# Kernel optimization log

Measured on AMD Instinct MI355X. Metric: run time of the kernel, lower is better.

The kernel has to match this reference:

```python
import jax, jax.numpy as jnp
import numpy as np

EMB_DIM = 256
ATTN_DIM = 64
B, K = 16384, 64


def setup_inputs() -> dict:
    key = jax.random.key(0)
    ks = jax.random.split(key, 7)
    center = jax.random.normal(ks[0], (B, EMB_DIM), dtype=jnp.float32)
    neigh_embs = jax.random.normal(ks[1], (B, K, EMB_DIM), dtype=jnp.float32)
    ppi_weights = jax.random.uniform(ks[2], (B, K), dtype=jnp.float32)
    # learned params (Linear stores weight as [out, in]; we keep that layout)
    Wq = jax.random.normal(ks[3], (ATTN_DIM, EMB_DIM), dtype=jnp.float32) / np.sqrt(EMB_DIM)
    Wk = jax.random.normal(ks[4], (ATTN_DIM, EMB_DIM), dtype=jnp.float32) / np.sqrt(EMB_DIM)
    # xavier_uniform for W_gate: limit = sqrt(6/(fan_in+fan_out))
    lim = np.sqrt(6.0 / (2 * EMB_DIM + EMB_DIM))
    Wgate = jax.random.uniform(ks[5], (EMB_DIM, 2 * EMB_DIM), minval=-lim, maxval=lim, dtype=jnp.float32)
    bgate = jnp.zeros((EMB_DIM,), dtype=jnp.float32)
    return {"center": center, "neigh_embs": neigh_embs, "ppi_weights": ppi_weights,
            "Wq": Wq, "Wk": Wk, "Wgate": Wgate, "bgate": bgate}


def reference(center, neigh_embs, ppi_weights, Wq, Wk, Wgate, bgate):
    scale = ATTN_DIM ** -0.5
    q = center @ Wq.T                                   # [B, a]
    k = jnp.einsum('bkd,ad->bka', neigh_embs, Wk)        # [B, K, a]
    logits = jnp.einsum('ba,bka->bk', q, k) * scale      # [B, K]
    attn = jax.nn.softmax(logits, axis=-1)
    attn = attn * ppi_weights
    attn = attn / (jnp.sum(attn, axis=-1, keepdims=True) + 1e-8)
    # dropout is identity in eval mode
    context = jnp.einsum('bk,bkd->bd', attn, neigh_embs)  # [B, D]
    gate = jax.nn.sigmoid(jnp.concatenate([center, context], axis=-1) @ Wgate.T + bgate)
    return gate * center + (1.0 - gate) * context
```

## Files before the change

kernel.cpp:

```cpp
#include <hip/hip_runtime.h>
#include <hip/hip_bf16.h>
#include <cstdint>

#define B_N 16384
#define KN 64
#define DN 256
#define AN 64
#define ROWS 4

typedef float f32x4 __attribute__((ext_vector_type(4)));
typedef float f32x2 __attribute__((ext_vector_type(2)));
typedef short s16x8 __attribute__((ext_vector_type(8)));

static __device__ inline unsigned int pk2(float a, float b) {
    __hip_bfloat162 h = __float22bfloat162_rn(make_float2(a, b));
    return *reinterpret_cast<unsigned int*>(&h);
}
static __device__ inline float bf_lo(unsigned int v) { return __uint_as_float(v << 16); }
static __device__ inline float bf_hi(unsigned int v) { return __uint_as_float(v & 0xFFFF0000u); }

__global__ __launch_bounds__(256) void prep_kernel(const float* __restrict__ Wq,
                                                   const float* __restrict__ Wk,
                                                   const float* __restrict__ Wgate,
                                                   float* __restrict__ M,
                                                   unsigned int* __restrict__ Wgb) {
    int blk = blockIdx.x;
    int t = threadIdx.x;
    if (blk < DN) {
        float acc = 0.f;
        #pragma unroll
        for (int a = 0; a < AN; ++a)
            acc += Wq[a * DN + blk] * Wk[a * DN + t];
        M[blk * DN + t] = acc;
    } else {
        int d = blk - DN;
        const float* src = Wgate + (size_t)d * (2 * DN);
        Wgb[(size_t)d * 256 + t] = pk2(src[2 * t], src[2 * t + 1]);
    }
}

__global__ __launch_bounds__(256) void qk_kernel(const float* __restrict__ center,
                                                 const float* __restrict__ M,
                                                 unsigned int* __restrict__ qkb) {
    __shared__ float xs[32 * DN];
    int r0 = blockIdx.x * 32;
    int tid = threadIdx.x;

    const float4* src = (const float4*)(center + (size_t)r0 * DN);
    float4* dst = (float4*)xs;
    #pragma unroll
    for (int i = 0; i < 8; ++i)
        dst[tid + 256 * i] = src[tid + 256 * i];
    __syncthreads();

    int ty = tid >> 5, tx = tid & 31;
    float acc[4][8];
    #pragma unroll
    for (int r = 0; r < 4; ++r)
        #pragma unroll
        for (int c = 0; c < 8; ++c) acc[r][c] = 0.f;

    for (int k4 = 0; k4 < DN; k4 += 4) {
        float4 xr[4];
        #pragma unroll
        for (int r = 0; r < 4; ++r)
            xr[r] = *(const float4*)(&xs[(ty * 4 + r) * DN + k4]);
        #pragma unroll
        for (int kk = 0; kk < 4; ++kk) {
            float4 ma = *(const float4*)(&M[(size_t)(k4 + kk) * DN + tx * 8]);
            float4 mb = *(const float4*)(&M[(size_t)(k4 + kk) * DN + tx * 8 + 4]);
            #pragma unroll
            for (int r = 0; r < 4; ++r) {
                float x = (&xr[r].x)[kk];
                acc[r][0] += x * ma.x; acc[r][1] += x * ma.y;
                acc[r][2] += x * ma.z; acc[r][3] += x * ma.w;
                acc[r][4] += x * mb.x; acc[r][5] += x * mb.y;
                acc[r][6] += x * mb.z; acc[r][7] += x * mb.w;
            }
        }
    }
    #pragma unroll
    for (int r = 0; r < 4; ++r) {
        size_t row = (size_t)(r0 + ty * 4 + r);
        uint4 o;
        o.x = pk2(acc[r][0], acc[r][1]);
        o.y = pk2(acc[r][2], acc[r][3]);
        o.z = pk2(acc[r][4], acc[r][5]);
        o.w = pk2(acc[r][6], acc[r][7]);
        *(uint4*)&qkb[row * 128 + tx * 4] = o;
    }
}

__global__ __launch_bounds__(256, 2) void attn_kernel(const float* __restrict__ neigh,
                                                      const unsigned int* __restrict__ qkb,
                                                      const float* __restrict__ ppi,
                                                      float* __restrict__ ctx) {
    __shared__ unsigned int sn[KN * 128];
    __shared__ unsigned int sqk[ROWS * 128];
    __shared__ float slog[KN];
    __shared__ float sattn[4][KN];

    const int tid = threadIdx.x;
    const int lane = tid & 63;
    const int wv = tid >> 6;
    const int b0 = blockIdx.x * ROWS;

    f32x4 rr[16];
    {
        const f32x4* t4 = (const f32x4*)(neigh + (size_t)b0 * (KN * DN));
        #pragma unroll
        for (int i = 0; i < 16; ++i)
            rr[i] = __builtin_nontemporal_load(t4 + tid + 256 * i);
    }

    ((uint2*)sqk)[tid] = ((const uint2*)(qkb + (size_t)b0 * 128))[tid];

    float pv[ROWS];
    #pragma unroll
    for (int r = 0; r < ROWS; ++r) pv[r] = ppi[(size_t)(b0 + r) * KN + lane];

    #pragma unroll
    for (int r = 0; r < ROWS; ++r) {
        if (r > 0) __syncthreads();

        {
            uint2* dst = (uint2*)sn;
            #pragma unroll
            for (int i = 0; i < 16; ++i)
                dst[tid + 256 * i] = make_uint2(pk2(rr[i].x, rr[i].y), pk2(rr[i].z, rr[i].w));
        }
        if (r < ROWS - 1) {
            const f32x4* n4 = (const f32x4*)(neigh + (size_t)(b0 + r + 1) * (KN * DN));
            #pragma unroll
            for (int i = 0; i < 16; ++i)
                rr[i] = __builtin_nontemporal_load(n4 + tid + 256 * i);
        }
        __syncthreads();

        {
            const int g = tid >> 2, j = tid & 3;
            float acc = 0.f;
            #pragma unroll
            for (int m = 0; m < 32; ++m) {
                int s = (m + g) & 31;
                int p = j + 4 * s;
                unsigned int nv = sn[g * 128 + p];
                unsigned int qv = sqk[r * 128 + p];
                acc += bf_lo(nv) * bf_lo(qv) + bf_hi(nv) * bf_hi(qv);
            }
            acc += __shfl_xor(acc, 1, 64);
            acc += __shfl_xor(acc, 2, 64);
            if (j == 0) slog[g] = acc;
        }
        __syncthreads();

        {
            float l = slog[lane] * 0.125f;
            float mx = l;
            #pragma unroll
            for (int off = 32; off >= 1; off >>= 1)
                mx = fmaxf(mx, __shfl_xor(mx, off, 64));
            float e = expf(l - mx);
            float se = e;
            #pragma unroll
            for (int off = 32; off >= 1; off >>= 1)
                se += __shfl_xor(se, off, 64);
            float t = (e / se) * pv[r];
            float st = t;
            #pragma unroll
            for (int off = 32; off >= 1; off >>= 1)
                st += __shfl_xor(st, off, 64);
            sattn[wv][lane] = t / (st + 1e-8f);
        }

        {
            const int w = tid >> 1;
            const int sh = (tid & 1) ? 0 : 16;
            float c = 0.f;
            #pragma unroll
            for (int k = 0; k < KN; ++k) {
                unsigned int nv = sn[k * 128 + w];
                float xv = __uint_as_float((nv << sh) & 0xFFFF0000u);
                c += sattn[wv][k] * xv;
            }
            __builtin_nontemporal_store(c, ctx + (size_t)(b0 + r) * DN + tid);
        }
    }
}

__global__ __launch_bounds__(256) void gate_kernel(const float* __restrict__ center,
                                                   const float* __restrict__ ctxw,
                                                   const unsigned int* __restrict__ Wgb,
                                                   const float* __restrict__ bgate,
                                                   float* __restrict__ out) {
    __shared__ unsigned int xsb[32 * 260];
    const int r0 = blockIdx.x * 32;
    const int tid = threadIdx.x;

    const float4* c4 = (const float4*)(center + (size_t)r0 * DN);
    const float4* x4 = (const float4*)(ctxw + (size_t)r0 * DN);
    #pragma unroll
    for (int i = 0; i < 8; ++i) {
        int idx = tid + 256 * i;
        int r = idx >> 6, c = idx & 63;
        float4 cv = c4[idx];
        float4 xv = x4[idx];
        *(uint2*)&xsb[r * 260 + 2 * c]       = make_uint2(pk2(cv.x, cv.y), pk2(cv.z, cv.w));
        *(uint2*)&xsb[r * 260 + 128 + 2 * c] = make_uint2(pk2(xv.x, xv.y), pk2(xv.z, xv.w));
    }
    __syncthreads();

    const int wave = tid >> 6, lane = tid & 63;
    const int l15 = lane & 15, lhi = lane >> 4;

    f32x4 acc[2][4];
    #pragma unroll
    for (int mt = 0; mt < 2; ++mt)
        #pragma unroll
        for (int nt = 0; nt < 4; ++nt)
            acc[mt][nt] = (f32x4){0.f, 0.f, 0.f, 0.f};

    #pragma unroll
    for (int ks = 0; ks < 16; ++ks) {
        s16x8 a0 = *(const s16x8*)&xsb[(l15)      * 260 + ks * 16 + lhi * 4];
        s16x8 a1 = *(const s16x8*)&xsb[(l15 + 16) * 260 + ks * 16 + lhi * 4];
        s16x8 b[4];
        #pragma unroll
        for (int nt = 0; nt < 4; ++nt) {
            int d = wave * 64 + nt * 16 + l15;
            b[nt] = *(const s16x8*)&Wgb[(size_t)d * 256 + ks * 16 + lhi * 4];
        }
        #pragma unroll
        for (int nt = 0; nt < 4; ++nt) {
            acc[0][nt] = __builtin_amdgcn_mfma_f32_16x16x32_bf16(a0, b[nt], acc[0][nt], 0, 0, 0);
            acc[1][nt] = __builtin_amdgcn_mfma_f32_16x16x32_bf16(a1, b[nt], acc[1][nt], 0, 0, 0);
        }
    }

    #pragma unroll
    for (int mt = 0; mt < 2; ++mt)
        #pragma unroll
        for (int nt = 0; nt < 4; ++nt) {
            int col = wave * 64 + nt * 16 + l15;
            float bg = bgate[col];
            #pragma unroll
            for (int reg = 0; reg < 4; ++reg) {
                int row = mt * 16 + lhi * 4 + reg;
                size_t gr = (size_t)(r0 + row);
                float z = acc[mt][nt][reg] + bg;
                float gt = 1.0f / (1.0f + expf(-z));
                float ce = center[gr * DN + col];
                float cx = ctxw[gr * DN + col];
                out[gr * DN + col] = gt * ce + (1.0f - gt) * cx;
            }
        }
}

extern "C" void kernel_launch(void* const* d_in, const int* in_sizes, int n_in,
                              void* d_out, int out_size, void* d_ws, size_t ws_size,
                              hipStream_t stream) {
    const float* center = (const float*)d_in[0];
    const float* neigh  = (const float*)d_in[1];
    const float* ppi    = (const float*)d_in[2];
    const float* Wq     = (const float*)d_in[3];
    const float* Wk     = (const float*)d_in[4];
    const float* Wgate  = (const float*)d_in[5];
    const float* bgate  = (const float*)d_in[6];
    float* out = (float*)d_out;

    char* ws = (char*)d_ws;
    float* M          = (float*)(ws);
    unsigned int* Wgb = (unsigned int*)(ws + 262144);
    unsigned int* qkb = (unsigned int*)(ws + 524288);
    float* ctx        = (float*)(ws + 524288 + 8388608);

    prep_kernel<<<dim3(512), dim3(256), 0, stream>>>(Wq, Wk, Wgate, M, Wgb);
    qk_kernel<<<dim3(B_N / 32), dim3(256), 0, stream>>>(center, M, qkb);
    attn_kernel<<<dim3(B_N / ROWS), dim3(256), 0, stream>>>(neigh, qkb, ppi, ctx);
    gate_kernel<<<dim3(B_N / 32), dim3(256), 0, stream>>>(center, ctx, Wgb, bgate, out);
}
```

Baseline: 255.5 us.

## Fuse gate GEMM into attention kernel to drop ctx round-trip

Merges the gate projection and blend into the attention kernel, keeping center and context rows in shared memory and running a bf16 MFMA on the 4-row tile. This removes the fp32 ctx write and re-read through global memory and one kernel launch. In exchange each 4-row block re-reads the full bf16 gate weight matrix from cache and uses only a quarter of each 16-row MFMA tile, adding shared memory pressure and redundant weight traffic.

```diff
diff --git a/kernel.cpp b/kernel.cpp
--- a/kernel.cpp
+++ b/kernel.cpp
@@ -91,14 +91,20 @@
     }
 }
 
-__global__ __launch_bounds__(256, 2) void attn_kernel(const float* __restrict__ neigh,
-                                                      const unsigned int* __restrict__ qkb,
-                                                      const float* __restrict__ ppi,
-                                                      float* __restrict__ ctx) {
+__global__ __launch_bounds__(256, 2) void attn_gate_kernel(const float* __restrict__ neigh,
+                                                           const unsigned int* __restrict__ qkb,
+                                                           const float* __restrict__ ppi,
+                                                           const float* __restrict__ center,
+                                                           const unsigned int* __restrict__ Wgb,
+                                                           const float* __restrict__ bgate,
+                                                           float* __restrict__ out) {
     __shared__ unsigned int sn[KN * 128];
     __shared__ unsigned int sqk[ROWS * 128];
     __shared__ float slog[KN];
     __shared__ float sattn[4][KN];
+    __shared__ float scen[ROWS * DN];
+    __shared__ float sctx[ROWS * DN];
+    __shared__ unsigned int sgt[ROWS * 260];
 
     const int tid = threadIdx.x;
     const int lane = tid & 63;
@@ -114,6 +120,7 @@
     }
 
     ((uint2*)sqk)[tid] = ((const uint2*)(qkb + (size_t)b0 * 128))[tid];
+    ((float4*)scen)[tid] = ((const float4*)(center + (size_t)b0 * DN))[tid];
 
     float pv[ROWS];
     #pragma unroll
@@ -183,77 +190,57 @@
                 float xv = __uint_as_float((nv << sh) & 0xFFFF0000u);
                 c += sattn[wv][k] * xv;
             }
-            __builtin_nontemporal_store(c, ctx + (size_t)(b0 + r) * DN + tid);
-        }
-    }
-}
-
-__global__ __launch_bounds__(256) void gate_kernel(const float* __restrict__ center,
-                                                   const float* __restrict__ ctxw,
-                                                   const unsigned int* __restrict__ Wgb,
-                                                   const float* __restrict__ bgate,
-                                                   float* __restrict__ out) {
-    __shared__ unsigned int xsb[32 * 260];
-    const int r0 = blockIdx.x * 32;
-    const int tid = threadIdx.x;
-
-    const float4* c4 = (const float4*)(center + (size_t)r0 * DN);
-    const float4* x4 = (const float4*)(ctxw + (size_t)r0 * DN);
-    #pragma unroll
-    for (int i = 0; i < 8; ++i) {
-        int idx = tid + 256 * i;
-        int r = idx >> 6, c = idx & 63;
-        float4 cv = c4[idx];
-        float4 xv = x4[idx];
-        *(uint2*)&xsb[r * 260 + 2 * c]       = make_uint2(pk2(cv.x, cv.y), pk2(cv.z, cv.w));
-        *(uint2*)&xsb[r * 260 + 128 + 2 * c] = make_uint2(pk2(xv.x, xv.y), pk2(xv.z, xv.w));
+            sctx[r * DN + tid] = c;
+        }
     }
     __syncthreads();
 
-    const int wave = tid >> 6, lane = tid & 63;
-    const int l15 = lane & 15, lhi = lane >> 4;
-
-    f32x4 acc[2][4];
-    #pragma unroll
-    for (int mt = 0; mt < 2; ++mt)
-        #pragma unroll
-        for (int nt = 0; nt < 4; ++nt)
-            acc[mt][nt] = (f32x4){0.f, 0.f, 0.f, 0.f};
-
-    #pragma unroll
-    for (int ks = 0; ks < 16; ++ks) {
-        s16x8 a0 = *(const s16x8*)&xsb[(l15)      * 260 + ks * 16 + lhi * 4];
-        s16x8 a1 = *(const s16x8*)&xsb[(l15 + 16) * 260 + ks * 16 + lhi * 4];
-        s16x8 b[4];
-        #pragma unroll
-        for (int nt = 0; nt < 4; ++nt) {
-            int d = wave * 64 + nt * 16 + l15;
-            b[nt] = *(const s16x8*)&Wgb[(size_t)d * 256 + ks * 16 + lhi * 4];
-        }
-        #pragma unroll
-        for (int nt = 0; nt < 4; ++nt) {
-            acc[0][nt] = __builtin_amdgcn_mfma_f32_16x16x32_bf16(a0, b[nt], acc[0][nt], 0, 0, 0);
-            acc[1][nt] = __builtin_amdgcn_mfma_f32_16x16x32_bf16(a1, b[nt], acc[1][nt], 0, 0, 0);
-        }
-    }
-
-    #pragma unroll
-    for (int mt = 0; mt < 2; ++mt)
-        #pragma unroll
-        for (int nt = 0; nt < 4; ++nt) {
-            int col = wave * 64 + nt * 16 + l15;
-            float bg = bgate[col];
-            #pragma unroll
-            for (int reg = 0; reg < 4; ++reg) {
-                int row = mt * 16 + lhi * 4 + reg;
-                size_t gr = (size_t)(r0 + row);
-                float z = acc[mt][nt][reg] + bg;
-                float gt = 1.0f / (1.0f + expf(-z));
-                float ce = center[gr * DN + col];
-                float cx = ctxw[gr * DN + col];
-                out[gr * DN + col] = gt * ce + (1.0f - gt) * cx;
-            }
-        }
+    #pragma unroll
+    for (int i = 0; i < 4; ++i) {
+        int w = tid + 256 * i;
+        int row = w >> 8, p = w & 255;
+        const float* srcrow = (p < 128) ? &scen[row * DN] : &sctx[row * DN];
+        int pp = (p & 127) * 2;
+        sgt[row * 260 + p] = pk2(srcrow[pp], srcrow[pp + 1]);
+    }
+    __syncthreads();
+
+    {
+        const int l15 = lane & 15, lhi = lane >> 4;
+        const int row4 = l15 & 3;
+
+        f32x4 acc[4];
+        #pragma unroll
+        for (int nt = 0; nt < 4; ++nt) acc[nt] = (f32x4){0.f, 0.f, 0.f, 0.f};
+
+        #pragma unroll
+        for (int ks = 0; ks < 16; ++ks) {
+            s16x8 a = *(const s16x8*)&sgt[row4 * 260 + ks * 16 + lhi * 4];
+            #pragma unroll
+            for (int nt = 0; nt < 4; ++nt) {
+                int d = wv * 64 + nt * 16 + l15;
+                s16x8 b = *(const s16x8*)&Wgb[(size_t)d * 256 + ks * 16 + lhi * 4];
+                acc[nt] = __builtin_amdgcn_mfma_f32_16x16x32_bf16(a, b, acc[nt], 0, 0, 0);
+            }
+        }
+
+        if (lhi == 0) {
+            #pragma unroll
+            for (int nt = 0; nt < 4; ++nt) {
+                int col = wv * 64 + nt * 16 + l15;
+                float bg = bgate[col];
+                #pragma unroll
+                for (int reg = 0; reg < 4; ++reg) {
+                    int row = reg;
+                    float z = acc[nt][reg] + bg;
+                    float gt = 1.0f / (1.0f + expf(-z));
+                    float ce = scen[row * DN + col];
+                    float cx = sctx[row * DN + col];
+                    out[(size_t)(b0 + row) * DN + col] = gt * ce + (1.0f - gt) * cx;
+                }
+            }
+        }
+    }
 }
 
 extern "C" void kernel_launch(void* const* d_in, const int* in_sizes, int n_in,
@@ -272,10 +259,9 @@
     float* M          = (float*)(ws);
     unsigned int* Wgb = (unsigned int*)(ws + 262144);
     unsigned int* qkb = (unsigned int*)(ws + 524288);
-    float* ctx        = (float*)(ws + 524288 + 8388608);
 
     prep_kernel<<<dim3(512), dim3(256), 0, stream>>>(Wq, Wk, Wgate, M, Wgb);
     qk_kernel<<<dim3(B_N / 32), dim3(256), 0, stream>>>(center, M, qkb);
-    attn_kernel<<<dim3(B_N / ROWS), dim3(256), 0, stream>>>(neigh, qkb, ppi, ctx);
-    gate_kernel<<<dim3(B_N / 32), dim3(256), 0, stream>>>(center, ctx, Wgb, bgate, out);
-}
+    attn_gate_kernel<<<dim3(B_N / ROWS), dim3(256), 0, stream>>>(neigh, qkb, ppi,
+                                                                 center, Wgb, bgate, out);
+}
```

New measurement: 315.8 us. 23.6% more time.
